# Optimization experiments

Hardware: AMD Instinct MI355X
Metric: run time of the kernel (lower is better)

Reference implementation:

```python
import jax, jax.numpy as jnp
import numpy as np

N_EMB = 1024
NUM_HEADS = 16
HEAD_DIM = N_EMB // NUM_HEADS
B, T = 4, 2048


def setup_inputs() -> dict:
    key = jax.random.key(0)
    k1, k2, k3, k4, k5 = jax.random.split(key, 5)
    s = 0.02
    return {
        "x": jax.random.normal(k1, (B, T, N_EMB), dtype=jnp.float32),
        "w_qkv": jax.random.normal(k2, (N_EMB, 3 * N_EMB), dtype=jnp.float32) * s,
        "b_qkv": jnp.zeros((3 * N_EMB,), dtype=jnp.float32),
        "w_proj": jax.random.normal(k3, (N_EMB, N_EMB), dtype=jnp.float32) * s,
        "b_proj": jnp.zeros((N_EMB,), dtype=jnp.float32),
    }


def reference(x, w_qkv, b_qkv, w_proj, b_proj):
    Bx, Tx, C = x.shape
    qkv = x @ w_qkv + b_qkv  # [B,T,3C]
    q, k, v = jnp.split(qkv, 3, axis=-1)
    # [B,H,T,D]
    def heads(t):
        return t.reshape(Bx, Tx, NUM_HEADS, HEAD_DIM).transpose(0, 2, 1, 3)
    q, k, v = heads(q), heads(k), heads(v)
    scale = 1.0 / np.sqrt(HEAD_DIM).astype(np.float32)
    att = jnp.einsum('bhqd,bhkd->bhqk', q, k) * scale
    causal = jnp.tril(jnp.ones((Tx, Tx), dtype=bool))
    att = jnp.where(causal[None, None], att, -jnp.inf)
    att = jax.nn.softmax(att, axis=-1)
    # dropout omitted (eval mode / deterministic reference)
    y = jnp.einsum('bhqk,bhkd->bhqd', att, v)
    y = y.transpose(0, 2, 1, 3).reshape(Bx, Tx, C)
    return y @ w_proj + b_proj
```

## Files before the change

kernel.cpp:

```cpp
#include <hip/hip_runtime.h>
#include <hip/hip_bf16.h>

typedef __attribute__((ext_vector_type(8))) short short8;
typedef __attribute__((ext_vector_type(4))) float f32x4;

static __device__ __forceinline__ unsigned short f2bf(float f) {
    unsigned int u = __builtin_bit_cast(unsigned int, f);
    u += 0x7fff + ((u >> 16) & 1);
    return (unsigned short)(u >> 16);
}

static __device__ __forceinline__ float bf2f(unsigned short u) {
    return __builtin_bit_cast(float, (unsigned int)u << 16);
}

static __device__ __forceinline__ void gl_lds16(const unsigned short* g, unsigned short* l) {
    __builtin_amdgcn_global_load_lds(
        (const __attribute__((address_space(1))) unsigned int*)g,
        (__attribute__((address_space(3))) unsigned int*)l, 16, 0, 0);
}

__global__ __launch_bounds__(256) void k_f32_to_bf16(
    const float* __restrict__ in, unsigned short* __restrict__ out, long n)
{
    long i = ((long)blockIdx.x * 256 + threadIdx.x) * 8;
    if (i >= n) return;
    const f32x4 a = *reinterpret_cast<const f32x4*>(in + i);
    const f32x4 b = *reinterpret_cast<const f32x4*>(in + i + 4);
    union { unsigned short u[8]; uint4 v; } o;
    o.u[0] = f2bf(a[0]); o.u[1] = f2bf(a[1]); o.u[2] = f2bf(a[2]); o.u[3] = f2bf(a[3]);
    o.u[4] = f2bf(b[0]); o.u[5] = f2bf(b[1]); o.u[6] = f2bf(b[2]); o.u[7] = f2bf(b[3]);
    *reinterpret_cast<uint4*>(out + i) = o.v;
}

__global__ __launch_bounds__(256) void k_transpose_w(
    const float* __restrict__ w, unsigned short* __restrict__ wt, int K, int N)
{
    __shared__ unsigned short tile[64][72];
    const int k0 = blockIdx.x * 64, n0 = blockIdx.y * 64;
    const int tid = threadIdx.x;
#pragma unroll
    for (int it = 0; it < 4; ++it) {
        int idx = it * 256 + tid;
        int kl = idx >> 4;
        int nl = (idx & 15) * 4;
        f32x4 v = *reinterpret_cast<const f32x4*>(w + (long)(k0 + kl) * N + n0 + nl);
        tile[kl][nl + 0] = f2bf(v[0]);
        tile[kl][nl + 1] = f2bf(v[1]);
        tile[kl][nl + 2] = f2bf(v[2]);
        tile[kl][nl + 3] = f2bf(v[3]);
    }
    __syncthreads();
#pragma unroll
    for (int it = 0; it < 2; ++it) {
        int idx = it * 256 + tid;
        int nl = idx >> 3;
        int c  = (idx & 7) * 8;
        union { unsigned short u[8]; uint4 v; } o;
#pragma unroll
        for (int j = 0; j < 8; ++j) o.u[j] = tile[c + j][nl];
        *reinterpret_cast<uint4*>(wt + (long)(n0 + nl) * K + k0 + c) = o.v;
    }
}

template <int OUTF32>
__global__ __launch_bounds__(256) void k_gemm_bt(
    const unsigned short* __restrict__ A,
    const unsigned short* __restrict__ Bt,
    const float* __restrict__ bias,
    void* __restrict__ Cv, int M, int N, int K)
{
    __shared__ unsigned short As[128][72];
    __shared__ unsigned short Bs[128][72];
    const int tid = threadIdx.x;
    const int m0 = blockIdx.x * 128;
    const int n0 = blockIdx.y * 128;
    const int w = tid >> 6, lane = tid & 63;
    const int wr = (w >> 1) * 64, wc = (w & 1) * 64;
    const int l4 = lane >> 4, l15 = lane & 15;

    f32x4 acc[4][4] = {};
    const int nk = K / 64;
    for (int kt = 0; kt < nk; ++kt) {
        const int k0 = kt * 64;
        __syncthreads();
#pragma unroll
        for (int it = 0; it < 4; ++it) {
            int idx = it * 256 + tid;
            int r = idx >> 3, c = (idx & 7) * 8;
            *reinterpret_cast<uint4*>(&As[r][c]) =
                *reinterpret_cast<const uint4*>(A + (long)(m0 + r) * K + k0 + c);
            *reinterpret_cast<uint4*>(&Bs[r][c]) =
                *reinterpret_cast<const uint4*>(Bt + (long)(n0 + r) * K + k0 + c);
        }
        __syncthreads();
#pragma unroll
        for (int kk = 0; kk < 2; ++kk) {
            short8 af[4], bf[4];
#pragma unroll
            for (int m = 0; m < 4; ++m)
                af[m] = *reinterpret_cast<const short8*>(&As[wr + m * 16 + l15][kk * 32 + l4 * 8]);
#pragma unroll
            for (int n = 0; n < 4; ++n)
                bf[n] = *reinterpret_cast<const short8*>(&Bs[wc + n * 16 + l15][kk * 32 + l4 * 8]);
#pragma unroll
            for (int m = 0; m < 4; ++m)
#pragma unroll
                for (int n = 0; n < 4; ++n)
                    acc[m][n] = __builtin_amdgcn_mfma_f32_16x16x32_bf16(af[m], bf[n], acc[m][n], 0, 0, 0);
        }
    }
#pragma unroll
    for (int n = 0; n < 4; ++n) {
        const int col = n0 + wc + n * 16 + l15;
        const float bv = bias[col];
#pragma unroll
        for (int m = 0; m < 4; ++m) {
            const int row = m0 + wr + m * 16 + l4 * 4;
#pragma unroll
            for (int i = 0; i < 4; ++i) {
                float v = acc[m][n][i] + bv;
                if (OUTF32)
                    reinterpret_cast<float*>(Cv)[(long)(row + i) * N + col] = v;
                else
                    reinterpret_cast<unsigned short*>(Cv)[(long)(row + i) * N + col] = f2bf(v);
            }
        }
    }
}

__global__ __launch_bounds__(256) void k_transpose_v(
    const unsigned short* __restrict__ qkv, unsigned short* __restrict__ vt, int T)
{
    __shared__ unsigned short tile[64][72];
    const int t0 = blockIdx.x * 64, bh = blockIdx.y;
    const int b = bh >> 4, h = bh & 15;
    const int tid = threadIdx.x;
#pragma unroll
    for (int it = 0; it < 2; ++it) {
        int idx = it * 256 + tid;
        int r = idx >> 3, c = (idx & 7) * 8;
        *reinterpret_cast<uint4*>(&tile[r][c]) =
            *reinterpret_cast<const uint4*>(qkv + (long)(b * T + t0 + r) * 3072 + 2048 + h * 64 + c);
    }
    __syncthreads();
#pragma unroll
    for (int it = 0; it < 2; ++it) {
        int idx = it * 256 + tid;
        int d = idx >> 3, c = (idx & 7) * 8;
        union { unsigned short u[8]; uint4 v; } o;
#pragma unroll
        for (int j = 0; j < 8; ++j) o.u[j] = tile[c + j][d];
        *reinterpret_cast<uint4*>(vt + ((long)bh * 64 + d) * T + t0 + c) = o.v;
    }
}

__global__ __launch_bounds__(256, 4) void k_attn(
    const unsigned short* __restrict__ qkv,
    const unsigned short* __restrict__ vt,
    unsigned short* __restrict__ y, int T)
{
    __shared__ __align__(16) unsigned short Kb[2][64][64];
    __shared__ __align__(16) unsigned short Vb[2][64][64];
    __shared__ __align__(16) unsigned short Ps[4][16][64];
    const int nQT = T >> 6;

    int n = blockIdx.x + gridDim.x * blockIdx.y;
    n = (n & 7) * ((gridDim.x * gridDim.y) >> 3) + (n >> 3);
    const int qa = n & 15;
    const int qb = nQT - 1 - qa;
    const int bh = n >> 4;
    const int b = bh >> 4, h = bh & 15;
    const int tid = threadIdx.x, w = tid >> 6, lane = tid & 63;
    const int l4 = lane >> 4, l15 = lane & 15;

    const float SC = 0.125f * 1.44269504f;

    const unsigned short* qpA = qkv + (long)(b * T + qa * 64 + w * 16 + l15) * 3072 + h * 64;
    const unsigned short* qpB = qkv + (long)(b * T + qb * 64 + w * 16 + l15) * 3072 + h * 64;
    short8 qfA[2], qfB[2];
    qfA[0] = *reinterpret_cast<const short8*>(qpA + l4 * 8);
    qfA[1] = *reinterpret_cast<const short8*>(qpA + 32 + l4 * 8);
    qfB[0] = *reinterpret_cast<const short8*>(qpB + l4 * 8);
    qfB[1] = *reinterpret_cast<const short8*>(qpB + 32 + l4 * 8);
#pragma unroll
    for (int kk = 0; kk < 2; ++kk)
#pragma unroll
        for (int j = 0; j < 8; ++j) {
            qfA[kk][j] = (short)f2bf(bf2f((unsigned short)qfA[kk][j]) * SC);
            qfB[kk][j] = (short)f2bf(bf2f((unsigned short)qfB[kk][j]) * SC);
        }

    short8 onesf;
#pragma unroll
    for (int j = 0; j < 8; ++j) onesf[j] = (short)0x3F80;

    const int lrow  = lane >> 3;
    const int lslot = (lane & 7) ^ lrow;
    const unsigned short* kg = qkv + (long)b * T * 3072 + 1024 + h * 64 + lslot * 8;
    const unsigned short* vg = vt + (long)bh * 64 * T + lslot * 8;

    auto stage = [&](int buf, int kt) {
#pragma unroll
        for (int i = 0; i < 2; ++i) {
            const int rb = (w * 2 + i) * 8;
            gl_lds16(kg + (long)(kt * 64 + rb + lrow) * 3072, &Kb[buf][rb][0]);
            gl_lds16(vg + (long)(rb + lrow) * T + kt * 64,    &Vb[buf][rb][0]);
        }
    };

    f32x4 oA[4] = {}, oB[4] = {};
    f32x4 lsA = {}, lsB = {};
    const int qcol = w * 16 + l15;
    const int pswz = (l15 & 7) << 3;
    int cur = 0;

    auto do_tile = [&](const short8 (&qf)[2], f32x4 (&o)[4], f32x4 &ls,
                       bool diag) {
        f32x4 s[4] = {};
        __builtin_amdgcn_s_setprio(1);
#pragma unroll
        for (int kk = 0; kk < 2; ++kk)
#pragma unroll
            for (int c = 0; c < 4; ++c) {
                const int r = c * 16 + l15;
                short8 kf = *reinterpret_cast<const short8*>(
                    &Kb[cur][r][(((kk * 4 + l4) ^ (r & 7)) * 8)]);
                s[c] = __builtin_amdgcn_mfma_f32_16x16x32_bf16(kf, qf[kk], s[c], 0, 0, 0);
            }
        __builtin_amdgcn_s_setprio(0);
#pragma unroll
        for (int c = 0; c < 4; ++c) {
            float p0 = exp2f(s[c][0]), p1 = exp2f(s[c][1]);
            float p2 = exp2f(s[c][2]), p3 = exp2f(s[c][3]);
            if (diag) {
                const int kl = c * 16 + l4 * 4;
                if (kl + 0 > qcol) p0 = 0.f;
                if (kl + 1 > qcol) p1 = 0.f;
                if (kl + 2 > qcol) p2 = 0.f;
                if (kl + 3 > qcol) p3 = 0.f;
            }
            unsigned int u01 = (__builtin_bit_cast(unsigned int, p1) & 0xffff0000u) |
                               (__builtin_bit_cast(unsigned int, p0) >> 16);
            unsigned int u23 = (__builtin_bit_cast(unsigned int, p3) & 0xffff0000u) |
                               (__builtin_bit_cast(unsigned int, p2) >> 16);
            const int colb = (c * 16 + l4 * 4) ^ pswz;
            *reinterpret_cast<uint2*>(&Ps[w][l15][colb]) = make_uint2(u01, u23);
        }
        __builtin_amdgcn_s_setprio(1);
#pragma unroll
        for (int kk = 0; kk < 2; ++kk) {
            short8 pf = *reinterpret_cast<const short8*>(
                &Ps[w][l15][(kk * 32 + l4 * 8) ^ pswz]);
            ls = __builtin_amdgcn_mfma_f32_16x16x32_bf16(pf, onesf, ls, 0, 0, 0);
#pragma unroll
            for (int nn = 0; nn < 4; ++nn) {
                const int r = nn * 16 + l15;
                short8 vf = *reinterpret_cast<const short8*>(
                    &Vb[cur][r][(((kk * 4 + l4) ^ (r & 7)) * 8)]);
                o[nn] = __builtin_amdgcn_mfma_f32_16x16x32_bf16(pf, vf, o[nn], 0, 0, 0);
            }
        }
        __builtin_amdgcn_s_setprio(0);
    };

    stage(0, 0);
    __syncthreads();
    for (int kt = 0; kt <= qb; ++kt) {
        if (kt < qb) stage(cur ^ 1, kt + 1);
        do_tile(qfB, oB, lsB, kt == qb);
        if (kt <= qa) do_tile(qfA, oA, lsA, kt == qa);
        __syncthreads();
        cur ^= 1;
    }

#pragma unroll
    for (int i = 0; i < 4; ++i) {
        float invA = 1.f / lsA[i];
        float invB = 1.f / lsB[i];
        int qArow = qa * 64 + w * 16 + l4 * 4 + i;
        int qBrow = qb * 64 + w * 16 + l4 * 4 + i;
        unsigned short* ypA = y + (long)(b * T + qArow) * 1024 + h * 64;
        unsigned short* ypB = y + (long)(b * T + qBrow) * 1024 + h * 64;
#pragma unroll
        for (int nn = 0; nn < 4; ++nn) {
            ypA[nn * 16 + l15] = f2bf(oA[nn][i] * invA);
            ypB[nn * 16 + l15] = f2bf(oB[nn][i] * invB);
        }
    }
}

extern "C" void kernel_launch(void* const* d_in, const int* in_sizes, int n_in,
                              void* d_out, int out_size, void* d_ws, size_t ws_size,
                              hipStream_t stream) {
    const float* x      = (const float*)d_in[0];
    const float* w_qkv  = (const float*)d_in[1];
    const float* b_qkv  = (const float*)d_in[2];
    const float* w_proj = (const float*)d_in[3];
    const float* b_proj = (const float*)d_in[4];
    float* out = (float*)d_out;

    const int B = 4, T = 2048, C = 1024, H = 16;
    const long M = (long)B * T;

    char* ws = (char*)d_ws;
    unsigned short* xb  = (unsigned short*)ws; ws += M * C * 2;
    unsigned short* wqt = (unsigned short*)ws; ws += (long)3 * C * C * 2;
    unsigned short* wpt = (unsigned short*)ws; ws += (long)C * C * 2;
    unsigned short* qkv = (unsigned short*)ws; ws += M * 3 * C * 2;
    unsigned short* vt  = (unsigned short*)ws; ws += M * C * 2;
    unsigned short* y   = (unsigned short*)ws; ws += M * C * 2;

    k_f32_to_bf16<<<(int)((M * C / 8 + 255) / 256), 256, 0, stream>>>(x, xb, M * C);
    {
        dim3 g(C / 64, 3 * C / 64);
        k_transpose_w<<<g, 256, 0, stream>>>(w_qkv, wqt, C, 3 * C);
    }
    {
        dim3 g(C / 64, C / 64);
        k_transpose_w<<<g, 256, 0, stream>>>(w_proj, wpt, C, C);
    }
    {
        dim3 g(M / 128, 3 * C / 128);
        k_gemm_bt<0><<<g, 256, 0, stream>>>(xb, wqt, b_qkv, qkv, (int)M, 3 * C, C);
    }
    {
        dim3 g(T / 64, B * H);
        k_transpose_v<<<g, 256, 0, stream>>>(qkv, vt, T);
    }
    {
        dim3 g(T / 128, B * H);
        k_attn<<<g, 256, 0, stream>>>(qkv, vt, y, T);
    }
    {
        dim3 g(M / 128, C / 128);
        k_gemm_bt<1><<<g, 256, 0, stream>>>(y, wpt, b_proj, out, (int)M, C, C);
    }
}
```

Before: 188.8 us.

## Double-buffer GEMM tiles via direct global-to-LDS loads with XOR swizzle

Replaces the register-staged global-to-LDS copy in the bf16 GEMM with direct global_load_lds transfers into two LDS buffers. The next K tile is prefetched while MFMAs run on the current one, and the padded layout becomes an XOR-swizzled 64-wide layout to avoid bank conflicts. The aim is to overlap memory latency with compute and remove one barrier per iteration. It doubles LDS use, which may lower occupancy, and correctness depends on the swizzle matching the wave-uniform LDS destination layout.

```diff
diff --git a/kernel.cpp b/kernel.cpp
--- a/kernel.cpp
+++ b/kernel.cpp
@@ -70,45 +70,54 @@
     const float* __restrict__ bias,
     void* __restrict__ Cv, int M, int N, int K)
 {
-    __shared__ unsigned short As[128][72];
-    __shared__ unsigned short Bs[128][72];
+    __shared__ __align__(16) unsigned short As[2][128][64];
+    __shared__ __align__(16) unsigned short Bs[2][128][64];
     const int tid = threadIdx.x;
     const int m0 = blockIdx.x * 128;
     const int n0 = blockIdx.y * 128;
     const int w = tid >> 6, lane = tid & 63;
     const int wr = (w >> 1) * 64, wc = (w & 1) * 64;
     const int l4 = lane >> 4, l15 = lane & 15;
+    const int lrow  = lane >> 3;
+    const int lslot = (lane & 7) ^ lrow;
+
+    auto stage = [&](int buf, int k0) {
+#pragma unroll
+        for (int it = 0; it < 4; ++it) {
+            const int rb = (w * 4 + it) * 8;
+            gl_lds16(A  + (long)(m0 + rb + lrow) * K + k0 + lslot * 8, &As[buf][rb][0]);
+            gl_lds16(Bt + (long)(n0 + rb + lrow) * K + k0 + lslot * 8, &Bs[buf][rb][0]);
+        }
+    };
 
     f32x4 acc[4][4] = {};
     const int nk = K / 64;
+    int cur = 0;
+    stage(0, 0);
+    __syncthreads();
     for (int kt = 0; kt < nk; ++kt) {
-        const int k0 = kt * 64;
-        __syncthreads();
-#pragma unroll
-        for (int it = 0; it < 4; ++it) {
-            int idx = it * 256 + tid;
-            int r = idx >> 3, c = (idx & 7) * 8;
-            *reinterpret_cast<uint4*>(&As[r][c]) =
-                *reinterpret_cast<const uint4*>(A + (long)(m0 + r) * K + k0 + c);
-            *reinterpret_cast<uint4*>(&Bs[r][c]) =
-                *reinterpret_cast<const uint4*>(Bt + (long)(n0 + r) * K + k0 + c);
-        }
-        __syncthreads();
+        if (kt + 1 < nk) stage(cur ^ 1, (kt + 1) * 64);
 #pragma unroll
         for (int kk = 0; kk < 2; ++kk) {
             short8 af[4], bf[4];
 #pragma unroll
-            for (int m = 0; m < 4; ++m)
-                af[m] = *reinterpret_cast<const short8*>(&As[wr + m * 16 + l15][kk * 32 + l4 * 8]);
-#pragma unroll
-            for (int n = 0; n < 4; ++n)
-                bf[n] = *reinterpret_cast<const short8*>(&Bs[wc + n * 16 + l15][kk * 32 + l4 * 8]);
+            for (int m = 0; m < 4; ++m) {
+                const int r = wr + m * 16 + l15;
+                af[m] = *reinterpret_cast<const short8*>(&As[cur][r][((kk * 4 + l4) ^ (r & 7)) * 8]);
+            }
+#pragma unroll
+            for (int n = 0; n < 4; ++n) {
+                const int r = wc + n * 16 + l15;
+                bf[n] = *reinterpret_cast<const short8*>(&Bs[cur][r][((kk * 4 + l4) ^ (r & 7)) * 8]);
+            }
 #pragma unroll
             for (int m = 0; m < 4; ++m)
 #pragma unroll
                 for (int n = 0; n < 4; ++n)
                     acc[m][n] = __builtin_amdgcn_mfma_f32_16x16x32_bf16(af[m], bf[n], acc[m][n], 0, 0, 0);
         }
+        __syncthreads();
+        cur ^= 1;
     }
 #pragma unroll
     for (int n = 0; n < 4; ++n) {
```

Result: faster. 180.0 us (-4.7%).
